# Kernel optimization log

Measured on AMD Instinct MI355X. Metric: run time of the kernel, lower is better.

## Reference

```python
import jax, jax.numpy as jnp
import numpy as np

DIM = 768
NUM_HEADS = 12
HEAD_DIM = DIM // NUM_HEADS
SCALE = HEAD_DIM ** -0.5


def setup_inputs() -> dict:
    key = jax.random.key(0)
    k1, k2, k3, k4 = jax.random.split(key, 4)
    B, N = 8, 1024
    x = jax.random.normal(k1, (B, N, DIM), dtype=jnp.float32)
    # qkv: Linear(dim, 3*dim, bias=False). Stored as [dim, 3*dim] (input-major).
    w_qkv = jax.random.normal(k2, (DIM, 3 * DIM), dtype=jnp.float32) * (DIM ** -0.5)
    # proj: Linear(dim, dim) with bias.
    w_proj = jax.random.normal(k3, (DIM, DIM), dtype=jnp.float32) * (DIM ** -0.5)
    b_proj = jax.random.normal(k4, (DIM,), dtype=jnp.float32) * 0.01
    return {"x": x, "w_qkv": w_qkv, "w_proj": w_proj, "b_proj": b_proj}


def reference(x, w_qkv, w_proj, b_proj):
    B, N, C = x.shape
    H, D = NUM_HEADS, HEAD_DIM
    qkv = (x @ w_qkv).reshape(B, N, 3, H, D)
    qkv = jnp.transpose(qkv, (2, 0, 3, 1, 4))
    q, k, v = qkv[0], qkv[1], qkv[2]
    # attention scores [B, H, N, N]
    attn = jnp.einsum("bhnd,bhmd->bhnm", q, k) * SCALE
    attn = jax.nn.softmax(attn, axis=-1)
    # weighted values -> [B, H, N, D] -> [B, N, C]
    out = jnp.einsum("bhnm,bhmd->bhnd", attn, v)
    out = jnp.transpose(out, (0, 2, 1, 3)).reshape(B, N, C)
    return out @ w_proj + b_proj
```

## Files before the change

### kernel.cpp

```cpp
#include <hip/hip_runtime.h>

#define BATCH 8
#define SEQ   1024
#define DIM   768
#define NH    12
#define HD    64
#define NTOK  (BATCH * SEQ)
#define QKVN  (3 * DIM)
#define QSCALE (0.125f * 1.44269504f)

typedef short bf8   __attribute__((ext_vector_type(8)));
typedef short bf4   __attribute__((ext_vector_type(4)));
typedef float f32x4 __attribute__((ext_vector_type(4)));
typedef int   i32x2 __attribute__((ext_vector_type(2)));
typedef int   i32x4 __attribute__((ext_vector_type(4)));

static __device__ __forceinline__ short f2bf(float f) {
    unsigned u = __float_as_uint(f);
    u += 0x7fffu + ((u >> 16) & 1u);
    return (short)(u >> 16);
}

static __device__ __forceinline__ int pack_bf16(float a, float b) {
    unsigned ua = __float_as_uint(a); ua += 0x7fffu + ((ua >> 16) & 1u);
    unsigned ub = __float_as_uint(b); ub += 0x7fffu + ((ub >> 16) & 1u);
    return (int)((ua >> 16) | (ub & 0xffff0000u));
}

static __device__ __forceinline__ float fast_exp2(float x) {
#if __has_builtin(__builtin_amdgcn_exp2f)
    return __builtin_amdgcn_exp2f(x);
#else
    return exp2f(x);
#endif
}

static __device__ __forceinline__ void gload_lds16(const short* g, short* l) {
    __builtin_amdgcn_global_load_lds(
        (const __attribute__((address_space(1))) void*)g,
        (__attribute__((address_space(3))) void*)l, 16, 0, 0);
}

__global__ __launch_bounds__(256) void convx_k(const float* __restrict__ in,
                                               short* __restrict__ out) {
    int i = blockIdx.x * 256 + threadIdx.x;
    f32x4 v = ((const f32x4*)in)[i];
    bf4 o;
    o[0] = f2bf(v[0]); o[1] = f2bf(v[1]); o[2] = f2bf(v[2]); o[3] = f2bf(v[3]);
    ((bf4*)out)[i] = o;
}

__global__ __launch_bounds__(256) void transpose_bf16_k(
        const float* __restrict__ in, short* __restrict__ out, int R, int C) {
    __shared__ short t[32][33];
    const int tx = threadIdx.x & 31;
    const int ty = threadIdx.x >> 5;
    const int c0 = blockIdx.x * 32;
    const int r0 = blockIdx.y * 32;
    #pragma unroll
    for (int i = 0; i < 32; i += 8)
        t[ty + i][tx] = f2bf(in[(size_t)(r0 + ty + i) * C + c0 + tx]);
    __syncthreads();
    #pragma unroll
    for (int i = 0; i < 32; i += 8)
        out[(size_t)(c0 + ty + i) * R + r0 + tx] = t[tx][ty + i];
}

static __device__ __forceinline__ void gemm_core_128(
        const short* __restrict__ A, const short* __restrict__ WT,
        int m0, int n0, int tid, short* aL, short* bL, f32x4 acc[4][4]) {
    const int lane = tid & 63;
    const int wid  = tid >> 6;
    const int ln   = lane & 15;
    const int quad = lane >> 4;
    const int wm = (wid >> 1) * 64;
    const int wn = (wid & 1) * 64;

    int rowx[4], colx[4];
    #pragma unroll
    for (int cc = 0; cc < 4; cc++) {
        int cf = (wid * 4 + cc) * 64 + lane;
        int r = cf >> 3;
        rowx[cc] = r;
        colx[cc] = (cf & 7) ^ (r & 7);
    }

    #pragma unroll
    for (int cc = 0; cc < 4; cc++) {
        const int dst = (wid * 4 + cc) * 512;
        gload_lds16(A  + (size_t)(m0 + rowx[cc]) * DIM + colx[cc] * 8, aL + dst);
        gload_lds16(WT + (size_t)(n0 + rowx[cc]) * DIM + colx[cc] * 8, bL + dst);
    }

    for (int it = 0; it < DIM / 64; it++) {
        const int cur = it & 1;
        __syncthreads();
        if (it + 1 < DIM / 64) {
            const int nb = (cur ^ 1) * 8192;
            const int kt = (it + 1) * 64;
            #pragma unroll
            for (int cc = 0; cc < 4; cc++) {
                const int dst = nb + (wid * 4 + cc) * 512;
                gload_lds16(A  + (size_t)(m0 + rowx[cc]) * DIM + kt + colx[cc] * 8, aL + dst);
                gload_lds16(WT + (size_t)(n0 + rowx[cc]) * DIM + kt + colx[cc] * 8, bL + dst);
            }
        }
        const int cb = cur * 8192;
        #pragma unroll
        for (int kc = 0; kc < 2; kc++) {
            const int sw = ((kc * 4 + quad) ^ (ln & 7)) * 8;
            bf8 af[4], bw[4];
            #pragma unroll
            for (int mi = 0; mi < 4; mi++)
                af[mi] = *(const bf8*)&aL[cb + (wm + mi * 16 + ln) * 64 + sw];
            #pragma unroll
            for (int ni = 0; ni < 4; ni++)
                bw[ni] = *(const bf8*)&bL[cb + (wn + ni * 16 + ln) * 64 + sw];
            #pragma unroll
            for (int mi = 0; mi < 4; mi++)
                #pragma unroll
                for (int ni = 0; ni < 4; ni++)
                    acc[mi][ni] = __builtin_amdgcn_mfma_f32_16x16x32_bf16(
                            af[mi], bw[ni], acc[mi][ni], 0, 0, 0);
        }
    }
}

static __device__ __forceinline__ void xcd_map(int id, int NX, int& xt, int& yt) {
    int r = id % (NX * 8);
    int g = id / (NX * 8);
    xt = r >> 3;
    yt = ((r & 7) << 3) + g;
}

__global__ __launch_bounds__(256) void gemm_qkv_k(
        const short* __restrict__ X, const short* __restrict__ WT,
        short* __restrict__ Qb, short* __restrict__ Kb, short* __restrict__ VT) {
    __shared__ short aL[2 * 128 * 64];
    __shared__ short bL[2 * 128 * 64];
    const int tid  = threadIdx.x;
    const int lane = tid & 63;
    const int wid  = tid >> 6;
    const int ln   = lane & 15;
    const int quad = lane >> 4;
    int xt, yt;
    xcd_map(blockIdx.x, QKVN / 128, xt, yt);
    const int m0 = yt * 128;
    const int n0 = xt * 128;
    const int wm = (wid >> 1) * 64;
    const int wn = (wid & 1) * 64;

    const f32x4 vzero = {0.f, 0.f, 0.f, 0.f};
    f32x4 acc[4][4];
    #pragma unroll
    for (int i = 0; i < 4; i++)
        #pragma unroll
        for (int j = 0; j < 4; j++) acc[i][j] = vzero;

    gemm_core_128(X, WT, m0, n0, tid, aL, bL, acc);

    const int b = m0 / SEQ;
    const int mt = m0 - b * SEQ;
    #pragma unroll
    for (int ni = 0; ni < 4; ni++) {
        const int nb = n0 + wn + ni * 16;
        const int three = nb / DIM;
        const int rem = nb - three * DIM;
        const int h = rem >> 6;
        const int d = (rem & 63) + ln;
        const size_t bh = (size_t)(b * NH + h);
        if (three < 2) {
            short* dst = (three == 0 ? Qb : Kb) + bh * SEQ * HD;
            const float scl = (three == 0) ? QSCALE : 1.0f;
            #pragma unroll
            for (int mi = 0; mi < 4; mi++) {
                #pragma unroll
                for (int r = 0; r < 4; r++) {
                    int tok = mt + wm + mi * 16 + quad * 4 + r;
                    dst[(size_t)tok * HD + d] = f2bf(acc[mi][ni][r] * scl);
                }
            }
        } else {
            short* dst = VT + bh * HD * SEQ + (size_t)d * SEQ;
            #pragma unroll
            for (int mi = 0; mi < 4; mi++) {
                int tok0 = mt + wm + mi * 16 + quad * 4;
                bf4 v;
                v[0] = f2bf(acc[mi][ni][0]); v[1] = f2bf(acc[mi][ni][1]);
                v[2] = f2bf(acc[mi][ni][2]); v[3] = f2bf(acc[mi][ni][3]);
                *(bf4*)&dst[tok0] = v;
            }
        }
    }
}

__global__ __launch_bounds__(256, 3) void attn_k(
        const short* __restrict__ Qb, const short* __restrict__ Kb,
        const short* __restrict__ VT, short* __restrict__ Ob) {
    __shared__ short kL[64 * 64];
    __shared__ short vL[64 * 64];
    const int tid  = threadIdx.x;
    const int lane = tid & 63;
    const int wid  = tid >> 6;
    const int ln   = lane & 15;
    const int quad = lane >> 4;
    const int bh = blockIdx.x;
    const int qt = blockIdx.y;
    const size_t base = (size_t)bh * SEQ * HD;
    const short* qg = Qb + base;
    const short* kg = Kb + base;
    const short* vg = VT + base;
    const int q0 = qt * 128 + wid * 32;

    int srow[2], scol[2];
    #pragma unroll
    for (int cc = 0; cc < 2; cc++) {
        int f = (wid * 2 + cc) * 64 + lane;
        int r = f >> 3;
        srow[cc] = r;
        scol[cc] = (f & 7) ^ (r & 7);
    }

    bf8 bq[2][2];
    #pragma unroll
    for (int qf = 0; qf < 2; qf++)
        #pragma unroll
        for (int kc = 0; kc < 2; kc++)
            bq[qf][kc] = *(const bf8*)&qg[(size_t)(q0 + qf * 16 + ln) * HD + kc * 32 + quad * 8];

    const f32x4 vzero = {0.f, 0.f, 0.f, 0.f};
    f32x4 o[2][4];
    #pragma unroll
    for (int qf = 0; qf < 2; qf++)
        #pragma unroll
        for (int c = 0; c < 4; c++) o[qf][c] = vzero;
    float l_lane[2] = {0.f, 0.f};

    for (int kt = 0; kt < SEQ; kt += 64) {
        __syncthreads();
        #pragma unroll
        for (int cc = 0; cc < 2; cc++) {
            const int dst = (wid * 2 + cc) * 512;
            gload_lds16(kg + (size_t)(kt + srow[cc]) * HD + scol[cc] * 8, kL + dst);
            gload_lds16(vg + (size_t)srow[cc] * SEQ + kt + scol[cc] * 8, vL + dst);
        }
        __syncthreads();

        bf8 ak[4][2];
        #pragma unroll
        for (int ng = 0; ng < 4; ng++)
            #pragma unroll
            for (int kc = 0; kc < 2; kc++)
                ak[ng][kc] = *(const bf8*)&kL[(ng * 16 + ln) * 64 + ((kc * 4 + quad) ^ (ln & 7)) * 8];
        bf8 bv[2][4];
        #pragma unroll
        for (int kch = 0; kch < 2; kch++)
            #pragma unroll
            for (int c = 0; c < 4; c++)
                bv[kch][c] = *(const bf8*)&vL[(c * 16 + ln) * 64 + ((kch * 4 + quad) ^ (ln & 7)) * 8];

        #pragma unroll
        for (int qf = 0; qf < 2; qf++) {
            #pragma unroll
            for (int kch = 0; kch < 2; kch++) {
                f32x4 s0 = __builtin_amdgcn_mfma_f32_16x16x32_bf16(ak[2 * kch][0], bq[qf][0], vzero, 0, 0, 0);
                s0 = __builtin_amdgcn_mfma_f32_16x16x32_bf16(ak[2 * kch][1], bq[qf][1], s0, 0, 0, 0);
                f32x4 s1 = __builtin_amdgcn_mfma_f32_16x16x32_bf16(ak[2 * kch + 1][0], bq[qf][0], vzero, 0, 0, 0);
                s1 = __builtin_amdgcn_mfma_f32_16x16x32_bf16(ak[2 * kch + 1][1], bq[qf][1], s1, 0, 0, 0);

                float e0[4], e1[4];
                #pragma unroll
                for (int r = 0; r < 4; r++) {
                    e0[r] = fast_exp2(s0[r]);
                    e1[r] = fast_exp2(s1[r]);
                    l_lane[qf] += e0[r] + e1[r];
                }
                int P0a = pack_bf16(e0[0], e0[1]);
                int P1a = pack_bf16(e0[2], e0[3]);
                int P0b = pack_bf16(e1[0], e1[1]);
                int P1b = pack_bf16(e1[2], e1[3]);
                i32x2 t0 = __builtin_amdgcn_permlane32_swap(P0a, P0b, false, false);
                i32x2 u0 = __builtin_amdgcn_permlane16_swap(t0[0], t0[1], false, false);
                i32x2 t1 = __builtin_amdgcn_permlane32_swap(P1a, P1b, false, false);
                i32x2 u1 = __builtin_amdgcn_permlane16_swap(t1[0], t1[1], false, false);
                i32x4 ai;
                ai[0] = u0[0]; ai[1] = u1[0]; ai[2] = u0[1]; ai[3] = u1[1];
                bf8 ap = __builtin_bit_cast(bf8, ai);

                #pragma unroll
                for (int c = 0; c < 4; c++)
                    o[qf][c] = __builtin_amdgcn_mfma_f32_16x16x32_bf16(
                            ap, bv[kch][c], o[qf][c], 0, 0, 0);
            }
        }
    }

    const int b = bh / NH;
    const int h = bh - b * NH;
    #pragma unroll
    for (int qf = 0; qf < 2; qf++) {
        float l = l_lane[qf];
        l += __shfl_xor(l, 16, 64);
        l += __shfl_xor(l, 32, 64);
        #pragma unroll
        for (int r = 0; r < 4; r++) {
            float inv = 1.0f / __shfl(l, quad * 4 + r, 64);
            int tok = q0 + qf * 16 + quad * 4 + r;
            size_t off = (size_t)(b * SEQ + tok) * DIM + h * HD;
            #pragma unroll
            for (int c = 0; c < 4; c++)
                Ob[off + c * 16 + ln] = f2bf(o[qf][c][r] * inv);
        }
    }
}

__global__ __launch_bounds__(256) void gemm_proj_k(
        const short* __restrict__ A, const short* __restrict__ WT,
        const float* __restrict__ bias, float* __restrict__ Out) {
    __shared__ short aL[2 * 128 * 64];
    __shared__ short bL[2 * 128 * 64];
    const int tid  = threadIdx.x;
    const int lane = tid & 63;
    const int ln   = lane & 15;
    const int quad = lane >> 4;
    const int wid  = tid >> 6;
    int xt, yt;
    xcd_map(blockIdx.x, DIM / 128, xt, yt);
    const int m0 = yt * 128;
    const int n0 = xt * 128;
    const int wm = (wid >> 1) * 64;
    const int wn = (wid & 1) * 64;

    const f32x4 vzero = {0.f, 0.f, 0.f, 0.f};
    f32x4 acc[4][4];
    #pragma unroll
    for (int i = 0; i < 4; i++)
        #pragma unroll
        for (int j = 0; j < 4; j++) acc[i][j] = vzero;

    gemm_core_128(A, WT, m0, n0, tid, aL, bL, acc);

    #pragma unroll
    for (int ni = 0; ni < 4; ni++) {
        int n = n0 + wn + ni * 16 + ln;
        float bi = bias[n];
        #pragma unroll
        for (int mi = 0; mi < 4; mi++) {
            #pragma unroll
            for (int r = 0; r < 4; r++) {
                int m = m0 + wm + mi * 16 + quad * 4 + r;
                Out[(size_t)m * DIM + n] = acc[mi][ni][r] + bi;
            }
        }
    }
}

extern "C" void kernel_launch(void* const* d_in, const int* in_sizes, int n_in,
                              void* d_out, int out_size, void* d_ws, size_t ws_size,
                              hipStream_t stream) {
    const float* x      = (const float*)d_in[0];
    const float* w_qkv  = (const float*)d_in[1];
    const float* w_proj = (const float*)d_in[2];
    const float* b_proj = (const float*)d_in[3];
    float* out = (float*)d_out;
    char* ws = (char*)d_ws;

    short* wqkvT  = (short*)(ws);
    short* wprojT = (short*)(ws +  3538944);
    short* qb     = (short*)(ws +  4718592);
    short* kb     = (short*)(ws + 17301504);
    short* vt     = (short*)(ws + 29884416);
    short* xb     = (short*)(ws + 42467328);
    short* attn   = xb;

    convx_k<<<dim3(NTOK * DIM / 1024), 256, 0, stream>>>(x, xb);
    transpose_bf16_k<<<dim3(QKVN / 32, DIM / 32), 256, 0, stream>>>(w_qkv, wqkvT, DIM, QKVN);
    transpose_bf16_k<<<dim3(DIM / 32, DIM / 32), 256, 0, stream>>>(w_proj, wprojT, DIM, DIM);
    gemm_qkv_k<<<dim3((QKVN / 128) * (NTOK / 128)), 256, 0, stream>>>(xb, wqkvT, qb, kb, vt);
    attn_k<<<dim3(BATCH * NH, SEQ / 128), 256, 0, stream>>>(qb, kb, vt, attn);
    gemm_proj_k<<<dim3((DIM / 128) * (NTOK / 128)), 256, 0, stream>>>(attn, wprojT, b_proj, out);
}
```

Baseline: 191.6 us.

## Double-buffer K/V tiles in attention and merge prep kernels into one launch

The attention loop now prefetches the next K/V tile into a second LDS buffer while computing on the current one, using a single barrier per iteration instead of two. The three preprocessing kernels (x conversion and two weight transposes) are merged into one launch dispatched by block index. This is meant to hide global-load latency in attention and cut launch overhead, at the cost of doubling attention LDS use, which may affect occupancy.

After: 192.2 us. No clear change (+0.3%).

```diff
diff --git a/kernel.cpp b/kernel.cpp
--- a/kernel.cpp
+++ b/kernel.cpp
@@ -41,22 +41,32 @@
         (__attribute__((address_space(3))) void*)l, 16, 0, 0);
 }
 
-__global__ __launch_bounds__(256) void convx_k(const float* __restrict__ in,
-                                               short* __restrict__ out) {
-    int i = blockIdx.x * 256 + threadIdx.x;
-    f32x4 v = ((const f32x4*)in)[i];
-    bf4 o;
-    o[0] = f2bf(v[0]); o[1] = f2bf(v[1]); o[2] = f2bf(v[2]); o[3] = f2bf(v[3]);
-    ((bf4*)out)[i] = o;
-}
-
-__global__ __launch_bounds__(256) void transpose_bf16_k(
-        const float* __restrict__ in, short* __restrict__ out, int R, int C) {
+__global__ __launch_bounds__(256) void prep_k(
+        const float* __restrict__ x, short* __restrict__ xb,
+        const float* __restrict__ wq, short* __restrict__ wqT,
+        const float* __restrict__ wp, short* __restrict__ wpT) {
+    const int id = blockIdx.x;
+    if (id < 6144) {
+        int i = id * 256 + threadIdx.x;
+        f32x4 v = ((const f32x4*)x)[i];
+        bf4 o;
+        o[0] = f2bf(v[0]); o[1] = f2bf(v[1]); o[2] = f2bf(v[2]); o[3] = f2bf(v[3]);
+        ((bf4*)xb)[i] = o;
+        return;
+    }
     __shared__ short t[32][33];
+    const float* in; short* out; int R, C, bx, by;
+    if (id < 7872) {
+        int k = id - 6144; bx = k % (QKVN / 32); by = k / (QKVN / 32);
+        in = wq; out = wqT; R = DIM; C = QKVN;
+    } else {
+        int k = id - 7872; bx = k % (DIM / 32); by = k / (DIM / 32);
+        in = wp; out = wpT; R = DIM; C = DIM;
+    }
     const int tx = threadIdx.x & 31;
     const int ty = threadIdx.x >> 5;
-    const int c0 = blockIdx.x * 32;
-    const int r0 = blockIdx.y * 32;
+    const int c0 = bx * 32;
+    const int r0 = by * 32;
     #pragma unroll
     for (int i = 0; i < 32; i += 8)
         t[ty + i][tx] = f2bf(in[(size_t)(r0 + ty + i) * C + c0 + tx]);
@@ -197,8 +207,8 @@
 __global__ __launch_bounds__(256, 3) void attn_k(
         const short* __restrict__ Qb, const short* __restrict__ Kb,
         const short* __restrict__ VT, short* __restrict__ Ob) {
-    __shared__ short kL[64 * 64];
-    __shared__ short vL[64 * 64];
+    __shared__ short kL[2 * 64 * 64];
+    __shared__ short vL[2 * 64 * 64];
     const int tid  = threadIdx.x;
     const int lane = tid & 63;
     const int wid  = tid >> 6;
@@ -236,28 +246,40 @@
         for (int c = 0; c < 4; c++) o[qf][c] = vzero;
     float l_lane[2] = {0.f, 0.f};
 
-    for (int kt = 0; kt < SEQ; kt += 64) {
+    #pragma unroll
+    for (int cc = 0; cc < 2; cc++) {
+        const int dst = (wid * 2 + cc) * 512;
+        gload_lds16(kg + (size_t)srow[cc] * HD + scol[cc] * 8, kL + dst);
+        gload_lds16(vg + (size_t)srow[cc] * SEQ + scol[cc] * 8, vL + dst);
+    }
+
+    for (int it = 0; it < SEQ / 64; it++) {
+        const int cur = it & 1;
         __syncthreads();
-        #pragma unroll
-        for (int cc = 0; cc < 2; cc++) {
-            const int dst = (wid * 2 + cc) * 512;
-            gload_lds16(kg + (size_t)(kt + srow[cc]) * HD + scol[cc] * 8, kL + dst);
-            gload_lds16(vg + (size_t)srow[cc] * SEQ + kt + scol[cc] * 8, vL + dst);
-        }
-        __syncthreads();
+        if (it + 1 < SEQ / 64) {
+            const int nb = (cur ^ 1) * 4096;
+            const int ktn = (it + 1) * 64;
+            #pragma unroll
+            for (int cc = 0; cc < 2; cc++) {
+                const int dst = nb + (wid * 2 + cc) * 512;
+                gload_lds16(kg + (size_t)(ktn + srow[cc]) * HD + scol[cc] * 8, kL + dst);
+                gload_lds16(vg + (size_t)srow[cc] * SEQ + ktn + scol[cc] * 8, vL + dst);
+            }
+        }
+        const int cb = cur * 4096;
 
         bf8 ak[4][2];
         #pragma unroll
         for (int ng = 0; ng < 4; ng++)
             #pragma unroll
             for (int kc = 0; kc < 2; kc++)
-                ak[ng][kc] = *(const bf8*)&kL[(ng * 16 + ln) * 64 + ((kc * 4 + quad) ^ (ln & 7)) * 8];
+                ak[ng][kc] = *(const bf8*)&kL[cb + (ng * 16 + ln) * 64 + ((kc * 4 + quad) ^ (ln & 7)) * 8];
         bf8 bv[2][4];
         #pragma unroll
         for (int kch = 0; kch < 2; kch++)
             #pragma unroll
             for (int c = 0; c < 4; c++)
-                bv[kch][c] = *(const bf8*)&vL[(c * 16 + ln) * 64 + ((kch * 4 + quad) ^ (ln & 7)) * 8];
+                bv[kch][c] = *(const bf8*)&vL[cb + (c * 16 + ln) * 64 + ((kch * 4 + quad) ^ (ln & 7)) * 8];
 
         #pragma unroll
         for (int qf = 0; qf < 2; qf++) {
@@ -373,9 +395,8 @@
     short* xb     = (short*)(ws + 42467328);
     short* attn   = xb;
 
-    convx_k<<<dim3(NTOK * DIM / 1024), 256, 0, stream>>>(x, xb);
-    transpose_bf16_k<<<dim3(QKVN / 32, DIM / 32), 256, 0, stream>>>(w_qkv, wqkvT, DIM, QKVN);
-    transpose_bf16_k<<<dim3(DIM / 32, DIM / 32), 256, 0, stream>>>(w_proj, wprojT, DIM, DIM);
+    prep_k<<<dim3(6144 + (QKVN / 32) * (DIM / 32) + (DIM / 32) * (DIM / 32)), 256, 0, stream>>>(
+            x, xb, w_qkv, wqkvT, w_proj, wprojT);
     gemm_qkv_k<<<dim3((QKVN / 128) * (NTOK / 128)), 256, 0, stream>>>(xb, wqkvT, qb, kb, vt);
     attn_k<<<dim3(BATCH * NH, SEQ / 128), 256, 0, stream>>>(qb, kb, vt, attn);
     gemm_proj_k<<<dim3((DIM / 128) * (NTOK / 128)), 256, 0, stream>>>(attn, wprojT, b_proj, out);
```
